# Performance work log

Hardware: AMD Instinct MI355X
Metric: run time of the kernel (lower is better)

The kernel has to match this reference:

```python
import jax, jax.numpy as jnp
import numpy as np

B, N, D = 2, 2048, 1024
H, DH = 16, 64  # heads, dim_head; dim_hidden = H*DH = 1024


def setup_inputs() -> dict:
    key = jax.random.key(0)
    ks = jax.random.split(key, 5)
    s = 0.02
    return {
        "x": jax.random.normal(ks[0], (B, N, D), dtype=jnp.float32),
        "W_w": jax.random.normal(ks[1], (3 * H * DH, D), dtype=jnp.float32) * s,
        "W_b": jax.random.normal(ks[2], (3 * H * DH,), dtype=jnp.float32) * s,
        "out_w": jax.random.normal(ks[3], (D, H * DH), dtype=jnp.float32) * s,
        "out_b": jax.random.normal(ks[4], (D,), dtype=jnp.float32) * s,
    }


def reference(x, W_w, W_b, out_w, out_b):
    b, n, _ = x.shape
    qkv = x @ W_w.T + W_b                       # [b, n, 3*H*DH]
    Q, K, V = jnp.split(qkv, 3, axis=-1)
    split_heads = lambda t: t.reshape(b, n, H, DH).transpose(0, 2, 1, 3)  # [b,h,n,dh]
    q, k, v = map(split_heads, (Q, K, V))
    scale = DH ** -0.5
    dots = jnp.einsum('bhik,bhjk->bhij', q, k) * scale   # [b,h,n,n]
    attn = jax.nn.softmax(dots, axis=-1)
    out = jnp.einsum('bhij,bhjk->bhik', attn, v)         # [b,h,n,dh]
    out = out.transpose(0, 2, 1, 3).reshape(b, n, H * DH)
    return out @ out_w.T + out_b
```

## Files before the change

### kernel.cpp

```cpp
#include <hip/hip_runtime.h>
#include <hip/hip_bf16.h>
#include <stdint.h>

#define BB 2
#define NN 2048
#define DD 1024
#define HH 16
#define DHD 64
#define MTOT (BB*NN)
#define QKVC (3*HH*DHD)

typedef unsigned short u16;
typedef __attribute__((ext_vector_type(8))) short short8;
typedef __attribute__((ext_vector_type(4))) float f32x4;
typedef __attribute__((ext_vector_type(16))) float f32x16;

#define QSCALE (0.125f * 1.44269504088896f)

#if __has_builtin(__builtin_amdgcn_exp2f)
#define EXP2(x) __builtin_amdgcn_exp2f(x)
#else
#define EXP2(x) exp2f(x)
#endif

static __device__ __forceinline__ u16 f2bf(float f) {
  union { float f; uint32_t u; } v; v.f = f;
  uint32_t r = (v.u + 0x7fffu + ((v.u >> 16) & 1u)) >> 16;
  return (u16)r;
}

static __device__ __forceinline__ uint32_t cvtpk_bf16(float lo, float hi) {
  uint32_t r;
  asm("v_cvt_pk_bf16_f32 %0, %1, %2" : "=v"(r) : "v"(lo), "v"(hi));
  return r;
}

static __device__ __forceinline__ float u2f(uint32_t u) {
  union { uint32_t u; float f; } v; v.u = u; return v.f;
}
static __device__ __forceinline__ uint32_t f2u(float f) {
  union { float f; uint32_t u; } v; v.f = f; return v.u;
}

static __device__ __forceinline__ void gload_lds16(const void* g, void* l) {
  __builtin_amdgcn_global_load_lds(
      (const __attribute__((address_space(1))) void*)g,
      (__attribute__((address_space(3))) void*)l, 16, 0, 0);
}

#define MFMA16(a, b, c) __builtin_amdgcn_mfma_f32_16x16x32_bf16((a), (b), (c), 0, 0, 0)
#define MFMA32(a, b, c) __builtin_amdgcn_mfma_f32_32x32x16_bf16((a), (b), (c), 0, 0, 0)

__global__ void k_cvt_all(const float* __restrict__ x, const float* __restrict__ Ww,
                          const float* __restrict__ ow,
                          u16* __restrict__ xb, u16* __restrict__ wwb, u16* __restrict__ owb) {
  int i = blockIdx.x * blockDim.x + threadIdx.x;
  const float* src; u16* dst; int off;
  if (i < 1048576)      { src = x;  dst = xb;  off = i; }
  else if (i < 1835008) { src = Ww; dst = wwb; off = i - 1048576; }
  else                  { src = ow; dst = owb; off = i - 1835008; }
  float4 v = ((const float4*)src)[off];
  ushort4 o;
  o.x = f2bf(v.x); o.y = f2bf(v.y); o.z = f2bf(v.z); o.w = f2bf(v.w);
  ((ushort4*)dst)[off] = o;
}

template<int EPI, int BM, int BN>
__global__ __launch_bounds__(256, EPI ? 4 : 3) void k_gemm_bt(
    const u16* __restrict__ A,
    const u16* __restrict__ Bm,
    const float* __restrict__ bias,
    u16* __restrict__ Qo, u16* __restrict__ Ko, u16* __restrict__ Vt,
    float* __restrict__ Co,
    int M, int NC, int K)
{
  constexpr int WM = BM / 2, WN = BN / 2;
  constexpr int FM = WM / 16, FN = WN / 16;
  __shared__ alignas(16) u16 As[2][BM * 32];
  __shared__ alignas(16) u16 Bs[2][BN * 32];
  const int t = threadIdx.x;
  const int lane = t & 63;
  const int wid = t >> 6;
  const int wr = wid >> 1, wc = wid & 1;
  const int l16 = lane & 15, lg = lane >> 4;
  const int col0 = blockIdx.x * BN;
  const int row0 = blockIdx.y * BM;

  f32x4 acc[FM][FN];
#pragma unroll
  for (int i = 0; i < FM; ++i)
#pragma unroll
    for (int j = 0; j < FN; ++j) acc[i][j] = (f32x4){0.f, 0.f, 0.f, 0.f};

  auto stage = [&](int buf, int tt) {
    const int kk = tt * 32;
#pragma unroll
    for (int i = 0; i < BM / 64; ++i) {
      int s = i * 256 + t;
      int r = s >> 2, c8 = (s & 3) * 8;
      gload_lds16(A + (size_t)(row0 + r) * K + kk + c8, ((char*)&As[buf][0]) + s * 16);
    }
#pragma unroll
    for (int i = 0; i < BN / 64; ++i) {
      int s = i * 256 + t;
      int r = s >> 2, c8 = (s & 3) * 8;
      gload_lds16(Bm + (size_t)(col0 + r) * K + kk + c8, ((char*)&Bs[buf][0]) + s * 16);
    }
  };

  auto compute = [&](int buf) {
    const u16* as = &As[buf][0];
    const u16* bs = &Bs[buf][0];
    short8 af[FM], bfr[FN];
#pragma unroll
    for (int i = 0; i < FM; ++i)
      af[i] = *(const short8*)&as[(wr * WM + i * 16 + l16) * 32 + lg * 8];
#pragma unroll
    for (int j = 0; j < FN; ++j)
      bfr[j] = *(const short8*)&bs[(wc * WN + j * 16 + l16) * 32 + lg * 8];
#pragma unroll
    for (int i = 0; i < FM; ++i)
#pragma unroll
      for (int j = 0; j < FN; ++j)
        acc[i][j] = MFMA16(af[i], bfr[j], acc[i][j]);
  };

  const int NT = K / 32;
  stage(0, 0);
  __syncthreads();
  int cur = 0;
  for (int tt = 0; tt < NT; ++tt) {
    if (tt + 1 < NT) stage(cur ^ 1, tt + 1);
    compute(cur);
    __syncthreads();
    cur ^= 1;
  }

  if (EPI == 1) {
#pragma unroll
    for (int j = 0; j < FN; ++j) {
      int col = col0 + wc * WN + j * 16 + l16;
      float bv = bias[col];
#pragma unroll
      for (int i = 0; i < FM; ++i) {
#pragma unroll
        for (int r = 0; r < 4; ++r) {
          int row = row0 + wr * WM + i * 16 + lg * 4 + r;
          Co[(size_t)row * NC + col] = acc[i][j][r] + bv;
        }
      }
    }
  } else {
#pragma unroll
    for (int j = 0; j < FN; ++j) {
      int col = col0 + wc * WN + j * 16 + l16;
      float bv = bias[col];
      int part = col >> 10, rem = col & 1023;
      int h = rem >> 6, dh = rem & 63;
#pragma unroll
      for (int i = 0; i < FM; ++i) {
        int rowb = row0 + wr * WM + i * 16 + lg * 4;
        int b = rowb >> 11;
        int nn = rowb & 2047;
        size_t bhN = (size_t)(b * HH + h) * NN;
        if (part == 0) {
#pragma unroll
          for (int r = 0; r < 4; ++r)
            Qo[(bhN + nn + r) * DHD + dh] = f2bf((acc[i][j][r] + bv) * QSCALE);
        } else if (part == 1) {
#pragma unroll
          for (int r = 0; r < 4; ++r) Ko[(bhN + nn + r) * DHD + dh] = f2bf(acc[i][j][r] + bv);
        } else {
          size_t base = ((size_t)(b * HH + h) * DHD + dh) * NN + nn;
          ushort4 pk;
          pk.x = f2bf(acc[i][j][0] + bv);
          pk.y = f2bf(acc[i][j][1] + bv);
          pk.z = f2bf(acc[i][j][2] + bv);
          pk.w = f2bf(acc[i][j][3] + bv);
          *(ushort4*)&Vt[base] = pk;
        }
      }
    }
  }
}

__global__ __launch_bounds__(256, 4) void k_gemm64(
    const u16* __restrict__ A,
    const u16* __restrict__ Bm,
    const float* __restrict__ bias, float* __restrict__ Co,
    int M, int NC, int K)
{
  __shared__ alignas(16) u16 As[2][64 * 64];
  __shared__ alignas(16) u16 Bs[2][64 * 64];
  const int t = threadIdx.x, lane = t & 63, wid = t >> 6;
  const int wr = wid >> 1, wc = wid & 1;
  const int l16 = lane & 15, lg = lane >> 4;
  const int col0 = blockIdx.x * 64, row0 = blockIdx.y * 64;

  f32x4 acc[2][2];
#pragma unroll
  for (int i = 0; i < 2; ++i)
#pragma unroll
    for (int j = 0; j < 2; ++j) acc[i][j] = (f32x4){0.f, 0.f, 0.f, 0.f};

  auto stage = [&](int buf, int tt) {
    const int kk = tt * 64;
#pragma unroll
    for (int i = 0; i < 2; ++i) {
      int s = i * 256 + t;
      int r = s >> 3, so = ((s & 7) * 16) ^ ((r & 7) << 4);
      gload_lds16((const char*)(A + (size_t)(row0 + r) * K + kk) + so,
                  ((char*)&As[buf][0]) + s * 16);
    }
#pragma unroll
    for (int i = 0; i < 2; ++i) {
      int s = i * 256 + t;
      int r = s >> 3, so = ((s & 7) * 16) ^ ((r & 7) << 4);
      gload_lds16((const char*)(Bm + (size_t)(col0 + r) * K + kk) + so,
                  ((char*)&Bs[buf][0]) + s * 16);
    }
  };

  auto compute = [&](int buf) {
    const char* as = (const char*)&As[buf][0];
    const char* bs = (const char*)&Bs[buf][0];
#pragma unroll
    for (int kkh = 0; kkh < 2; ++kkh) {
      short8 af[2], bfr[2];
#pragma unroll
      for (int i = 0; i < 2; ++i) {
        int row = wr * 32 + i * 16 + l16;
        af[i] = *(const short8*)(as + row * 128 + ((kkh * 64 + lg * 16) ^ ((row & 7) << 4)));
      }
#pragma unroll
      for (int j = 0; j < 2; ++j) {
        int row = wc * 32 + j * 16 + l16;
        bfr[j] = *(const short8*)(bs + row * 128 + ((kkh * 64 + lg * 16) ^ ((row & 7) << 4)));
      }
#pragma unroll
      for (int i = 0; i < 2; ++i)
#pragma unroll
        for (int j = 0; j < 2; ++j)
          acc[i][j] = MFMA16(af[i], bfr[j], acc[i][j]);
    }
  };

  const int NT = K / 64;
  stage(0, 0);
  __syncthreads();
  int cur = 0;
  for (int tt = 0; tt < NT; ++tt) {
    if (tt + 1 < NT) stage(cur ^ 1, tt + 1);
    compute(cur);
    __syncthreads();
    cur ^= 1;
  }

#pragma unroll
  for (int j = 0; j < 2; ++j) {
    int col = col0 + wc * 32 + j * 16 + l16;
    float bv = bias[col];
#pragma unroll
    for (int i = 0; i < 2; ++i)
#pragma unroll
      for (int r = 0; r < 4; ++r) {
        int row = row0 + wr * 32 + i * 16 + lg * 4 + r;
        Co[(size_t)row * NC + col] = acc[i][j][r] + bv;
      }
  }
}

__global__ __launch_bounds__(512, 4) void k_attn(
    const u16* __restrict__ Q, const u16* __restrict__ Kb,
    const u16* __restrict__ Vt, u16* __restrict__ AO)
{
  __shared__ alignas(16) char smem[65536];
  const int t = threadIdx.x, lane = t & 63, w = t >> 6;
  const int g = w >> 2, wg = w & 3;
  const int l32 = lane & 31, hi = lane >> 5;
  const int bid = blockIdx.x;
  const int xcd = bid & 7;
  const int idx = bid >> 3;
  const int bh = xcd * 4 + (idx >> 4);
  const int qt = idx & 15;
  const int b = bh >> 4, h = bh & 15;

  const u16* Qp  = Q + (size_t)bh * NN * DHD;
  const char* Kp = (const char*)(Kb + (size_t)bh * NN * DHD);
  const char* Vp = (const char*)(Vt + (size_t)bh * DHD * NN);

  const int q0 = qt * 128 + wg * 32;

  short8 qf[4];
#pragma unroll
  for (int kk = 0; kk < 4; ++kk)
    qf[kk] = *(const short8*)&Qp[(size_t)(q0 + l32) * DHD + kk * 16 + hi * 8];

  f32x16 oacc[2];
  oacc[0] = (f32x16)(0.f);
  oacc[1] = (f32x16)(0.f);
  float lsv[4] = {0.f, 0.f, 0.f, 0.f};

  char* gbase = smem + g * 32768;
  const int kvbase = g * 1024;

  const int srow = lane >> 3;
  const int scolb = (lane & 7) * 16;
  auto stage = [&](int buf, int kv) {
    char* base = gbase + buf * 16384;
#pragma unroll
    for (int i = 0; i < 2; ++i) {
      int r = wg * 16 + i * 8 + srow;
      gload_lds16(Kp + (size_t)(kv + r) * 128 + (scolb ^ ((r & 7) << 4)),
                  base + wg * 2048 + i * 1024 + lane * 16);
    }
#pragma unroll
    for (int i = 0; i < 2; ++i) {
      int r = wg * 16 + i * 8 + srow;
      gload_lds16(Vp + (size_t)r * (NN * 2) + (size_t)kv * 2 + (scolb ^ ((r & 7) << 4)),
                  base + 8192 + wg * 2048 + i * 1024 + lane * 16);
    }
  };

  auto subtile = [&](const char* bufK, const char* bufV, int sub) {
    const int krow = sub * 32 + l32;
    const char* kro = bufK + krow * 128;
    const int ksw = (krow & 7) << 4;
    short8 kf[4];
#pragma unroll
    for (int kk = 0; kk < 4; ++kk)
      kf[kk] = *(const short8*)(kro + ((kk * 32 + hi * 16) ^ ksw));

    f32x16 s = (f32x16)(0.f);
#pragma unroll
    for (int kk = 0; kk < 4; ++kk) s = MFMA32(kf[kk], qf[kk], s);

    float p[16];
#pragma unroll
    for (int r = 0; r < 16; ++r) p[r] = EXP2(s[r]);
#pragma unroll
    for (int r = 0; r < 16; ++r) lsv[r & 3] += p[r];

#pragma unroll
    for (int gs = 0; gs < 2; ++gs) {
      const int bix = gs * 8;
      uint32_t lo01 = cvtpk_bf16(p[bix + 0], p[bix + 1]);
      uint32_t lo23 = cvtpk_bf16(p[bix + 2], p[bix + 3]);
      uint32_t hi01 = cvtpk_bf16(p[bix + 4], p[bix + 5]);
      uint32_t hi23 = cvtpk_bf16(p[bix + 6], p[bix + 7]);
      auto ra = __builtin_amdgcn_permlane32_swap(lo01, hi01, false, false);
      auto rb = __builtin_amdgcn_permlane32_swap(lo23, hi23, false, false);
      union { uint32_t u[4]; short8 v; } pf;
      pf.u[0] = ra[0]; pf.u[1] = rb[0]; pf.u[2] = ra[1]; pf.u[3] = rb[1];
#pragma unroll
      for (int d = 0; d < 2; ++d) {
        const int vrow = d * 32 + l32;
        short8 vf = *(const short8*)(bufV + vrow * 128 +
                      ((sub * 64 + gs * 32 + hi * 16) ^ ((vrow & 7) << 4)));
        oacc[d] = MFMA32(vf, pf.v, oacc[d]);
      }
    }
  };

  const int NT = 16;
  stage(0, kvbase);
  asm volatile("s_waitcnt vmcnt(0)");
  __syncthreads();
  for (int t2 = 0; t2 < NT; ++t2) {
    int cur = t2 & 1;
    if (t2 + 1 < NT) stage(cur ^ 1, kvbase + (t2 + 1) * 64);
    const char* bK = gbase + cur * 16384;
    const char* bV = bK + 8192;
    subtile(bK, bV, 0);
    subtile(bK, bV, 1);
    asm volatile("s_waitcnt vmcnt(0)");
    __syncthreads();
  }

  float ls = (lsv[0] + lsv[1]) + (lsv[2] + lsv[3]);
  {
    auto rr = __builtin_amdgcn_permlane32_swap(f2u(ls), f2u(ls), false, false);
    ls = u2f(rr[0]) + u2f(rr[1]);
  }
  float* lsarea = (float*)smem;
  float* oarea  = (float*)(smem + 32768);
  if (g == 1) {
    lsarea[wg * 64 + lane] = ls;
    float* dst = oarea + (size_t)(wg * 64 + lane) * 32;
#pragma unroll
    for (int d = 0; d < 2; ++d)
#pragma unroll
      for (int i = 0; i < 4; ++i)
        ((f32x4*)dst)[d * 4 + i] = (f32x4){oacc[d][i*4+0], oacc[d][i*4+1],
                                           oacc[d][i*4+2], oacc[d][i*4+3]};
  }
  __syncthreads();
  if (g == 1) return;

  float lst = ls + lsarea[wg * 64 + lane];
  {
    const float* src = oarea + (size_t)(wg * 64 + lane) * 32;
#pragma unroll
    for (int d = 0; d < 2; ++d)
#pragma unroll
      for (int i = 0; i < 4; ++i) {
        f32x4 v = ((const f32x4*)src)[d * 4 + i];
        oacc[d][i*4+0] += v[0]; oacc[d][i*4+1] += v[1];
        oacc[d][i*4+2] += v[2]; oacc[d][i*4+3] += v[3];
      }
  }

  u16* olw = (u16*)(smem + 1024) + (size_t)wg * 32 * 72;
  float inv = 1.0f / lst;
#pragma unroll
  for (int d = 0; d < 2; ++d) {
#pragma unroll
    for (int i = 0; i < 8; ++i) {
      int r0 = 2 * i;
      int dh = d * 32 + (r0 & 3) + 8 * (r0 >> 2) + 4 * hi;
      uint32_t pk = cvtpk_bf16(oacc[d][r0] * inv, oacc[d][r0 + 1] * inv);
      *(uint32_t*)&olw[l32 * 72 + dh] = pk;
    }
  }
  __builtin_amdgcn_s_waitcnt(0);
#pragma unroll
  for (int rr = 0; rr < 4; ++rr) {
    int row = rr * 8 + (lane >> 3);
    short8 v = *(const short8*)&olw[row * 72 + (lane & 7) * 8];
    int n = q0 + row;
    *(short8*)&AO[((size_t)b * NN + n) * DD + h * DHD + (lane & 7) * 8] = v;
  }
}

extern "C" void kernel_launch(void* const* d_in, const int* in_sizes, int n_in,
                              void* d_out, int out_size, void* d_ws, size_t ws_size,
                              hipStream_t stream) {
  const float* x  = (const float*)d_in[0];
  const float* Ww = (const float*)d_in[1];
  const float* Wb = (const float*)d_in[2];
  const float* ow = (const float*)d_in[3];
  const float* ob = (const float*)d_in[4];
  float* out = (float*)d_out;

  char* ws = (char*)d_ws;
  u16* xb  = (u16*)(ws);
  u16* wwb = (u16*)(ws + ((size_t)8  << 20));
  u16* owb = (u16*)(ws + ((size_t)14 << 20));
  u16* Qb  = (u16*)(ws + ((size_t)16 << 20));
  u16* Kb  = (u16*)(ws + ((size_t)24 << 20));
  u16* Vt  = (u16*)(ws + ((size_t)32 << 20));
  u16* AO  = (u16*)(ws + ((size_t)40 << 20));

  k_cvt_all<<<8192, 256, 0, stream>>>(x, Ww, ow, xb, wwb, owb);

  dim3 g1(QKVC / 128, MTOT / 128);
  k_gemm_bt<0, 128, 128><<<g1, 256, 0, stream>>>(xb, wwb, Wb, Qb, Kb, Vt, nullptr, MTOT, QKVC, DD);

  k_attn<<<512, 512, 0, stream>>>(Qb, Kb, Vt, AO);

  dim3 g3(DD / 64, MTOT / 64);
  k_gemm64<<<g3, 256, 0, stream>>>(AO, owb, ob, out, MTOT, DD, DD);
}
```

Before: 108.7 us.

## Split K across two warp groups in output projection GEMM with LDS reduction

The output projection GEMM now launches 512 threads per block. Two groups of four waves each handle half of the K dimension, with their own double-buffered LDS tiles. Partial accumulators from the second group are written to shared memory and summed by the first group before the bias add and store. This halves the serial K loop per block and doubles the waves available to hide latency. In exchange it uses more LDS per block (64KB plus 16KB), which may reduce occupancy, and adds a reduction step.

After: 111.4 us. 2.6% more time.

```diff
diff --git a/kernel.cpp b/kernel.cpp
--- a/kernel.cpp
+++ b/kernel.cpp
@@ -184,18 +184,23 @@
   }
 }
 
-__global__ __launch_bounds__(256, 4) void k_gemm64(
+__global__ __launch_bounds__(512, 4) void k_gemm64ks(
     const u16* __restrict__ A,
     const u16* __restrict__ Bm,
     const float* __restrict__ bias, float* __restrict__ Co,
     int M, int NC, int K)
 {
-  __shared__ alignas(16) u16 As[2][64 * 64];
-  __shared__ alignas(16) u16 Bs[2][64 * 64];
-  const int t = threadIdx.x, lane = t & 63, wid = t >> 6;
+  __shared__ alignas(16) u16 As[2][2][64 * 64];
+  __shared__ alignas(16) u16 Bs[2][2][64 * 64];
+  __shared__ alignas(16) float carea[256 * 16];
+  const int t512 = threadIdx.x;
+  const int g = t512 >> 8;
+  const int t = t512 & 255;
+  const int lane = t & 63, wid = t >> 6;
   const int wr = wid >> 1, wc = wid & 1;
   const int l16 = lane & 15, lg = lane >> 4;
   const int col0 = blockIdx.x * 64, row0 = blockIdx.y * 64;
+  const int kbase = g * (K / 2);
 
   f32x4 acc[2][2];
 #pragma unroll
@@ -204,26 +209,26 @@
     for (int j = 0; j < 2; ++j) acc[i][j] = (f32x4){0.f, 0.f, 0.f, 0.f};
 
   auto stage = [&](int buf, int tt) {
-    const int kk = tt * 64;
+    const int kk = kbase + tt * 64;
 #pragma unroll
     for (int i = 0; i < 2; ++i) {
       int s = i * 256 + t;
       int r = s >> 3, so = ((s & 7) * 16) ^ ((r & 7) << 4);
       gload_lds16((const char*)(A + (size_t)(row0 + r) * K + kk) + so,
-                  ((char*)&As[buf][0]) + s * 16);
+                  ((char*)&As[g][buf][0]) + s * 16);
     }
 #pragma unroll
     for (int i = 0; i < 2; ++i) {
       int s = i * 256 + t;
       int r = s >> 3, so = ((s & 7) * 16) ^ ((r & 7) << 4);
       gload_lds16((const char*)(Bm + (size_t)(col0 + r) * K + kk) + so,
-                  ((char*)&Bs[buf][0]) + s * 16);
+                  ((char*)&Bs[g][buf][0]) + s * 16);
     }
   };
 
   auto compute = [&](int buf) {
-    const char* as = (const char*)&As[buf][0];
-    const char* bs = (const char*)&Bs[buf][0];
+    const char* as = (const char*)&As[g][buf][0];
+    const char* bs = (const char*)&Bs[g][buf][0];
 #pragma unroll
     for (int kkh = 0; kkh < 2; ++kkh) {
       short8 af[2], bfr[2];
@@ -245,7 +250,7 @@
     }
   };
 
-  const int NT = K / 64;
+  const int NT = K / 128;
   stage(0, 0);
   __syncthreads();
   int cur = 0;
@@ -254,6 +259,28 @@
     compute(cur);
     __syncthreads();
     cur ^= 1;
+  }
+
+  if (g == 1) {
+    float* dst = &carea[t * 16];
+#pragma unroll
+    for (int i = 0; i < 2; ++i)
+#pragma unroll
+      for (int j = 0; j < 2; ++j)
+        *(f32x4*)&dst[(i * 2 + j) * 4] = acc[i][j];
+  }
+  __syncthreads();
+  if (g == 1) return;
+  {
+    const float* src = &carea[t * 16];
+#pragma unroll
+    for (int i = 0; i < 2; ++i)
+#pragma unroll
+      for (int j = 0; j < 2; ++j) {
+        f32x4 v = *(const f32x4*)&src[(i * 2 + j) * 4];
+        acc[i][j][0] += v[0]; acc[i][j][1] += v[1];
+        acc[i][j][2] += v[2]; acc[i][j][3] += v[3];
+      }
   }
 
 #pragma unroll
@@ -459,5 +486,5 @@
   k_attn<<<512, 512, 0, stream>>>(Qb, Kb, Vt, AO);
 
   dim3 g3(DD / 64, MTOT / 64);
-  k_gemm64<<<g3, 256, 0, stream>>>(AO, owb, ob, out, MTOT, DD, DD);
-}
+  k_gemm64ks<<<g3, 512, 0, stream>>>(AO, owb, ob, out, MTOT, DD, DD);
+}
```
